# Kernel tuning notes

Measured on AMD Instinct MI355X. Metric: run time of the kernel, lower is better.

The kernel has to match this reference:

```python
import jax, jax.numpy as jnp
import numpy as np

PAD_IDX = 0
NUM_CODES = 100000
DIM = 16
B, L = 200000, 64


def setup_inputs() -> dict:
    key = jax.random.key(0)
    k1, k2 = jax.random.split(key)
    code_ids = jax.random.randint(k1, (B, L), 0, NUM_CODES, dtype=jnp.int32)
    emb_weight = jax.random.normal(k2, (NUM_CODES, DIM), dtype=jnp.float32)
    return {"code_ids": code_ids, "emb_weight": emb_weight}


def reference(code_ids, emb_weight):
    # mask of non-pad codes: [B, L]
    mask = (code_ids != PAD_IDX)
    # gather embeddings: [B, L, D] (pad rows gathered too, then zeroed by mask)
    gathered = emb_weight[code_ids]
    maskf = mask.astype(emb_weight.dtype)[..., None]          # [B, L, 1]
    summed = jnp.sum(gathered * maskf, axis=1)                 # [B, D]
    count = jnp.sum(mask, axis=1).astype(emb_weight.dtype)     # [B]
    denom = jnp.maximum(count, 1.0)[:, None]                   # avoid div-by-0
    # rows with zero valid codes -> zero vector (matches torch.zeros branch)
    return summed / denom
```

## Files before the change

kernel.cpp:

```cpp
#include <hip/hip_runtime.h>
#include <hip/hip_bf16.h>

#define PAD_IDX 0
#define DIM 16
#define SEQ_L 64
#define ROWS_PER_BLOCK 64
#define THREADS 256
#define ROW_STRIDE4 17

__device__ __forceinline__ float bf16_lo(unsigned int w) {
    return __uint_as_float(w << 16);
}
__device__ __forceinline__ float bf16_hi(unsigned int w) {
    return __uint_as_float(w & 0xffff0000u);
}

__global__ __launch_bounds__(THREADS) void convert_bf16_kernel(
    const float* __restrict__ emb, ushort* __restrict__ tab, int n )
{
    int i4 = (blockIdx.x * THREADS + threadIdx.x) * 4;
    if (i4 + 3 < n) {
        float4 v = *reinterpret_cast<const float4*>(emb + i4);
        ushort4 o;
        o.x = __bfloat16_as_ushort(__float2bfloat16(v.x));
        o.y = __bfloat16_as_ushort(__float2bfloat16(v.y));
        o.z = __bfloat16_as_ushort(__float2bfloat16(v.z));
        o.w = __bfloat16_as_ushort(__float2bfloat16(v.w));
        *reinterpret_cast<ushort4*>(tab + i4) = o;
    } else if (i4 < n) {
        for (int k = i4; k < n; ++k)
            tab[k] = __bfloat16_as_ushort(__float2bfloat16(emb[k]));
    }
}

__global__ __launch_bounds__(THREADS) void visit_encoder_bf16_kernel(
    const int* __restrict__ code_ids,
    const uint2* __restrict__ tab,
    float* __restrict__ out,
    int B, int n_codes4)
{
    __shared__ int4 lcodes[ROWS_PER_BLOCK * ROW_STRIDE4];

    const int t = threadIdx.x;
    const int block_row0 = blockIdx.x * ROWS_PER_BLOCK;

    const int4* src4 = reinterpret_cast<const int4*>(code_ids);
    const int base4 = blockIdx.x * (ROWS_PER_BLOCK * SEQ_L / 4);
    #pragma unroll
    for (int k = 0; k < 4; ++k) {
        int j = t + THREADS * k;
        int gj = base4 + j;
        if (gj >= n_codes4) gj = n_codes4 - 1;
        int4 v = src4[gj];
        lcodes[(j >> 4) * ROW_STRIDE4 + (j & 15)] = v;
    }
    __syncthreads();

    const int r  = t >> 2;
    const int d4 = t & 3;
    const uint2* tbase = tab + d4;

    float4 acc = make_float4(0.f, 0.f, 0.f, 0.f);
    int cnt = 0;

    #pragma unroll
    for (int l4 = 0; l4 < 16; l4 += 2) {
        int4 ca = lcodes[r * ROW_STRIDE4 + l4];
        int4 cb = lcodes[r * ROW_STRIDE4 + l4 + 1];
        int cs[8] = {ca.x, ca.y, ca.z, ca.w, cb.x, cb.y, cb.z, cb.w};
        uint2 e[8];
        #pragma unroll
        for (int u = 0; u < 8; ++u) {
            e[u] = tbase[(size_t)cs[u] * 4];
        }
        #pragma unroll
        for (int u = 0; u < 8; ++u) {
            float m = (cs[u] != PAD_IDX) ? 1.0f : 0.0f;
            acc.x = fmaf(bf16_lo(e[u].x), m, acc.x);
            acc.y = fmaf(bf16_hi(e[u].x), m, acc.y);
            acc.z = fmaf(bf16_lo(e[u].y), m, acc.z);
            acc.w = fmaf(bf16_hi(e[u].y), m, acc.w);
            cnt += (cs[u] != PAD_IDX);
        }
    }

    const int row = block_row0 + r;
    if (row < B) {
        float inv = 1.0f / fmaxf((float)cnt, 1.0f);
        float4 o;
        o.x = acc.x * inv; o.y = acc.y * inv; o.z = acc.z * inv; o.w = acc.w * inv;
        reinterpret_cast<float4*>(out)[(size_t)row * 4 + d4] = o;
    }
}

__global__ __launch_bounds__(THREADS) void visit_encoder_f32_kernel(
    const int* __restrict__ code_ids,
    const float* __restrict__ emb,
    float* __restrict__ out,
    int B, int n_codes4)
{
    __shared__ int4 lcodes[ROWS_PER_BLOCK * ROW_STRIDE4];
    const int t = threadIdx.x;
    const int block_row0 = blockIdx.x * ROWS_PER_BLOCK;
    const int4* src4 = reinterpret_cast<const int4*>(code_ids);
    const int base4 = blockIdx.x * (ROWS_PER_BLOCK * SEQ_L / 4);
    #pragma unroll
    for (int k = 0; k < 4; ++k) {
        int j = t + THREADS * k;
        int gj = base4 + j;
        if (gj >= n_codes4) gj = n_codes4 - 1;
        int4 v = src4[gj];
        lcodes[(j >> 4) * ROW_STRIDE4 + (j & 15)] = v;
    }
    __syncthreads();

    const int r  = t >> 2;
    const int d4 = t & 3;
    const float4* ebase = reinterpret_cast<const float4*>(emb) + d4;
    float4 acc = make_float4(0.f, 0.f, 0.f, 0.f);
    int cnt = 0;
    #pragma unroll
    for (int l4 = 0; l4 < 16; l4 += 2) {
        int4 ca = lcodes[r * ROW_STRIDE4 + l4];
        int4 cb = lcodes[r * ROW_STRIDE4 + l4 + 1];
        int cs[8] = {ca.x, ca.y, ca.z, ca.w, cb.x, cb.y, cb.z, cb.w};
        float4 e[8];
        #pragma unroll
        for (int u = 0; u < 8; ++u) e[u] = ebase[(size_t)cs[u] * 4];
        #pragma unroll
        for (int u = 0; u < 8; ++u) {
            float m = (cs[u] != PAD_IDX) ? 1.0f : 0.0f;
            acc.x = fmaf(e[u].x, m, acc.x);
            acc.y = fmaf(e[u].y, m, acc.y);
            acc.z = fmaf(e[u].z, m, acc.z);
            acc.w = fmaf(e[u].w, m, acc.w);
            cnt += (cs[u] != PAD_IDX);
        }
    }
    const int row = block_row0 + r;
    if (row < B) {
        float inv = 1.0f / fmaxf((float)cnt, 1.0f);
        float4 o;
        o.x = acc.x * inv; o.y = acc.y * inv; o.z = acc.z * inv; o.w = acc.w * inv;
        reinterpret_cast<float4*>(out)[(size_t)row * 4 + d4] = o;
    }
}

extern "C" void kernel_launch(void* const* d_in, const int* in_sizes, int n_in,
                              void* d_out, int out_size, void* d_ws, size_t ws_size,
                              hipStream_t stream) {
    const int*   code_ids = (const int*)d_in[0];
    const float* emb      = (const float*)d_in[1];
    float*       out      = (float*)d_out;

    const int total_codes = in_sizes[0];
    const int B = total_codes / SEQ_L;
    const int n_codes4 = total_codes / 4;
    const int emb_elems = in_sizes[1];
    const int grid = (B + ROWS_PER_BLOCK - 1) / ROWS_PER_BLOCK;

    const size_t tab_bytes = (size_t)emb_elems * sizeof(ushort);
    if (ws_size >= tab_bytes) {
        ushort* tab = (ushort*)d_ws;
        int n4 = (emb_elems + 3) / 4;
        convert_bf16_kernel<<<dim3((n4 + THREADS - 1) / THREADS), dim3(THREADS), 0, stream>>>(
            emb, tab, emb_elems);
        visit_encoder_bf16_kernel<<<dim3(grid), dim3(THREADS), 0, stream>>>(
            code_ids, (const uint2*)tab, out, B, n_codes4);
    } else {
        visit_encoder_f32_kernel<<<dim3(grid), dim3(THREADS), 0, stream>>>(
            code_ids, emb, out, B, n_codes4);
    }
}
```

Before: 68.58 us.

## Gather 16-byte bf16 halves per thread with 128 rows per block

```diff
diff --git a/kernel.cpp b/kernel.cpp
--- a/kernel.cpp
+++ b/kernel.cpp
@@ -2,11 +2,14 @@
 #include <hip/hip_bf16.h>
 
 #define PAD_IDX 0
-#define DIM 16
 #define SEQ_L 64
-#define ROWS_PER_BLOCK 64
+#define ROWS_PER_BLOCK 128
 #define THREADS 256
 #define ROW_STRIDE4 17
+
+typedef int   v4i __attribute__((ext_vector_type(4)));
+typedef uint  v4u __attribute__((ext_vector_type(4)));
+typedef float v4f __attribute__((ext_vector_type(4)));
 
 __device__ __forceinline__ float bf16_lo(unsigned int w) {
     return __uint_as_float(w << 16);
@@ -33,53 +36,60 @@
     }
 }
 
-__global__ __launch_bounds__(THREADS) void visit_encoder_bf16_kernel(
+__global__ __launch_bounds__(THREADS) void visit_encoder_bf16v2_kernel(
     const int* __restrict__ code_ids,
-    const uint2* __restrict__ tab,
+    const v4u* __restrict__ tab,
     float* __restrict__ out,
     int B, int n_codes4)
 {
-    __shared__ int4 lcodes[ROWS_PER_BLOCK * ROW_STRIDE4];
+    __shared__ v4i lcodes[ROWS_PER_BLOCK * ROW_STRIDE4];
 
     const int t = threadIdx.x;
     const int block_row0 = blockIdx.x * ROWS_PER_BLOCK;
 
-    const int4* src4 = reinterpret_cast<const int4*>(code_ids);
+    const v4i* src4 = reinterpret_cast<const v4i*>(code_ids);
     const int base4 = blockIdx.x * (ROWS_PER_BLOCK * SEQ_L / 4);
     #pragma unroll
-    for (int k = 0; k < 4; ++k) {
+    for (int k = 0; k < 8; ++k) {
         int j = t + THREADS * k;
         int gj = base4 + j;
         if (gj >= n_codes4) gj = n_codes4 - 1;
-        int4 v = src4[gj];
+        v4i v = __builtin_nontemporal_load(src4 + gj);
         lcodes[(j >> 4) * ROW_STRIDE4 + (j & 15)] = v;
     }
     __syncthreads();
 
-    const int r  = t >> 2;
-    const int d4 = t & 3;
-    const uint2* tbase = tab + d4;
+    const int r  = t >> 1;
+    const int d8 = t & 1;
+    const v4u* tbase = tab + d8;
 
-    float4 acc = make_float4(0.f, 0.f, 0.f, 0.f);
+    float acc[8] = {0.f,0.f,0.f,0.f,0.f,0.f,0.f,0.f};
     int cnt = 0;
 
     #pragma unroll
-    for (int l4 = 0; l4 < 16; l4 += 2) {
-        int4 ca = lcodes[r * ROW_STRIDE4 + l4];
-        int4 cb = lcodes[r * ROW_STRIDE4 + l4 + 1];
-        int cs[8] = {ca.x, ca.y, ca.z, ca.w, cb.x, cb.y, cb.z, cb.w};
-        uint2 e[8];
+    for (int b = 0; b < 4; ++b) {
+        int cs[16];
         #pragma unroll
-        for (int u = 0; u < 8; ++u) {
-            e[u] = tbase[(size_t)cs[u] * 4];
+        for (int q = 0; q < 4; ++q) {
+            v4i c4 = lcodes[r * ROW_STRIDE4 + b * 4 + q];
+            cs[q*4+0] = c4.x; cs[q*4+1] = c4.y; cs[q*4+2] = c4.z; cs[q*4+3] = c4.w;
+        }
+        v4u e[16];
+        #pragma unroll
+        for (int u = 0; u < 16; ++u) {
+            e[u] = tbase[(size_t)cs[u] * 2];
         }
         #pragma unroll
-        for (int u = 0; u < 8; ++u) {
+        for (int u = 0; u < 16; ++u) {
             float m = (cs[u] != PAD_IDX) ? 1.0f : 0.0f;
-            acc.x = fmaf(bf16_lo(e[u].x), m, acc.x);
-            acc.y = fmaf(bf16_hi(e[u].x), m, acc.y);
-            acc.z = fmaf(bf16_lo(e[u].y), m, acc.z);
-            acc.w = fmaf(bf16_hi(e[u].y), m, acc.w);
+            acc[0] = fmaf(bf16_lo(e[u].x), m, acc[0]);
+            acc[1] = fmaf(bf16_hi(e[u].x), m, acc[1]);
+            acc[2] = fmaf(bf16_lo(e[u].y), m, acc[2]);
+            acc[3] = fmaf(bf16_hi(e[u].y), m, acc[3]);
+            acc[4] = fmaf(bf16_lo(e[u].z), m, acc[4]);
+            acc[5] = fmaf(bf16_hi(e[u].z), m, acc[5]);
+            acc[6] = fmaf(bf16_lo(e[u].w), m, acc[6]);
+            acc[7] = fmaf(bf16_hi(e[u].w), m, acc[7]);
             cnt += (cs[u] != PAD_IDX);
         }
     }
@@ -87,9 +97,12 @@
     const int row = block_row0 + r;
     if (row < B) {
         float inv = 1.0f / fmaxf((float)cnt, 1.0f);
-        float4 o;
-        o.x = acc.x * inv; o.y = acc.y * inv; o.z = acc.z * inv; o.w = acc.w * inv;
-        reinterpret_cast<float4*>(out)[(size_t)row * 4 + d4] = o;
+        v4f o0, o1;
+        o0.x = acc[0]*inv; o0.y = acc[1]*inv; o0.z = acc[2]*inv; o0.w = acc[3]*inv;
+        o1.x = acc[4]*inv; o1.y = acc[5]*inv; o1.z = acc[6]*inv; o1.w = acc[7]*inv;
+        v4f* op = reinterpret_cast<v4f*>(out + (size_t)row * 16 + d8 * 8);
+        __builtin_nontemporal_store(o0, op);
+        __builtin_nontemporal_store(o1, op + 1);
     }
 }
 
@@ -99,21 +112,19 @@
     float* __restrict__ out,
     int B, int n_codes4)
 {
-    __shared__ int4 lcodes[ROWS_PER_BLOCK * ROW_STRIDE4];
+    __shared__ int4 lcodes[64 * ROW_STRIDE4];
     const int t = threadIdx.x;
-    const int block_row0 = blockIdx.x * ROWS_PER_BLOCK;
+    const int block_row0 = blockIdx.x * 64;
     const int4* src4 = reinterpret_cast<const int4*>(code_ids);
-    const int base4 = blockIdx.x * (ROWS_PER_BLOCK * SEQ_L / 4);
+    const int base4 = blockIdx.x * (64 * SEQ_L / 4);
     #pragma unroll
     for (int k = 0; k < 4; ++k) {
         int j = t + THREADS * k;
         int gj = base4 + j;
         if (gj >= n_codes4) gj = n_codes4 - 1;
-        int4 v = src4[gj];
-        lcodes[(j >> 4) * ROW_STRIDE4 + (j & 15)] = v;
+        lcodes[(j >> 4) * ROW_STRIDE4 + (j & 15)] = src4[gj];
     }
     __syncthreads();
-
     const int r  = t >> 2;
     const int d4 = t & 3;
     const float4* ebase = reinterpret_cast<const float4*>(emb) + d4;
@@ -157,7 +168,6 @@
     const int B = total_codes / SEQ_L;
     const int n_codes4 = total_codes / 4;
     const int emb_elems = in_sizes[1];
-    const int grid = (B + ROWS_PER_BLOCK - 1) / ROWS_PER_BLOCK;
 
     const size_t tab_bytes = (size_t)emb_elems * sizeof(ushort);
     if (ws_size >= tab_bytes) {
@@ -165,9 +175,11 @@
         int n4 = (emb_elems + 3) / 4;
         convert_bf16_kernel<<<dim3((n4 + THREADS - 1) / THREADS), dim3(THREADS), 0, stream>>>(
             emb, tab, emb_elems);
-        visit_encoder_bf16_kernel<<<dim3(grid), dim3(THREADS), 0, stream>>>(
-            code_ids, (const uint2*)tab, out, B, n_codes4);
+        const int grid = (B + ROWS_PER_BLOCK - 1) / ROWS_PER_BLOCK;
+        visit_encoder_bf16v2_kernel<<<dim3(grid), dim3(THREADS), 0, stream>>>(
+            code_ids, (const v4u*)tab, out, B, n_codes4);
     } else {
+        const int grid = (B + 63) / 64;
         visit_encoder_f32_kernel<<<dim3(grid), dim3(THREADS), 0, stream>>>(
             code_ids, emb, out, B, n_codes4);
     }
```

After: 78.35 us. 14.2% more time.
